# Performance work log

Measured on AMD Instinct MI355X. Metric: run time of the kernel, lower is better.

## Reference

```python
import jax, jax.numpy as jnp
import numpy as np

STEP, LEAK = 16, 32
KS = STEP + LEAK          # kernel_size = 48
FODEP = KS                # forced depression window
SYNAPSES, NEURONS = 64, 256
IC, OC = 1, 10
DENSE = 0.5
THETA = DENSE * SYNAPSES * IC   # 32.0
BIAS = 0.5
BATCH, TIME = 16, 512


def setup_inputs() -> dict:
    key = jax.random.key(0)
    k1, k2 = jax.random.split(key)
    # binary input spikes, density 0.2
    input_spikes = (jax.random.uniform(k1, (BATCH, IC, SYNAPSES, TIME)) < 0.2).astype(jnp.float32)
    # weight ~ Exponential(rate=1/w_init=2).sample().clip(0,1), mean 0.5
    u = jax.random.uniform(k2, (OC * NEURONS, IC * SYNAPSES), minval=1e-6, maxval=1.0)
    weight = jnp.clip(-0.5 * jnp.log(u), 0.0, 1.0)
    return {"input_spikes": input_spikes, "weight": weight}


def _step_fire_leak_kernel(weight):
    # kernel[o, i, t] = max(0, min(t/step, -(t - w*step)/leak + w)), flipped on t
    t = jnp.arange(KS, dtype=weight.dtype)
    t_spike = t / STEP                                        # rising edge
    t_leak = -(t - weight[..., None] * STEP) / LEAK + weight[..., None]  # decaying edge
    kernel = jnp.maximum(jnp.zeros((), weight.dtype), jnp.minimum(t_spike, t_leak))
    return kernel[..., ::-1]


def _forward(input_spikes, weight):
    B, C, S, T = input_spikes.shape
    x = input_spikes.reshape(B, C * S, T)
    kernel = _step_fire_leak_kernel(weight)                   # [OC*N, IC*S, KS]
    # conv1d with padding = kernel_size on both sides -> T' = T + KS + 1
    pot = jax.lax.conv_general_dilated(
        x, kernel, window_strides=(1,), padding=[(KS, KS)],
        dimension_numbers=("NCH", "OIH", "NCH"))
    Tp = pot.shape[-1]
    pot = pot.reshape(B, OC, NEURONS, Tp) + BIAS * THETA      # unsupervised bias path

    # winner-takes-all scan over time with per-(batch, neuron) depression counter
    pot_t = pot.transpose(3, 0, 2, 1)                         # [T', B, N, OC]
    dep0 = jnp.zeros((B, NEURONS, OC), jnp.int32)

    def step_fn(dep, p):
        masked = jnp.where(dep == 0, p, jnp.zeros((), p.dtype))
        winner = jnp.argmax(masked, axis=-1)                  # [B, N]
        wpot = jnp.take_along_axis(masked, winner[..., None], axis=-1)[..., 0]
        spike = (wpot > THETA).astype(p.dtype)                # [B, N]
        w_t = jax.nn.one_hot(winner, OC, dtype=p.dtype) * spike[..., None]
        dep = jnp.clip(dep + spike.astype(jnp.int32)[..., None] * FODEP - 1, 0, FODEP - 1)
        return dep, w_t

    _, winners = jax.lax.scan(step_fn, dep0, pot_t)           # [T', B, N, OC]
    return winners.transpose(1, 3, 2, 0)                      # [B, OC, N, T'] float


def reference(input_spikes, weight):
    return _forward(input_spikes, weight)
```

## Files before the change

### kernel.cpp

```cpp
#include <hip/hip_runtime.h>

#define B_   16
#define OC_  10
#define N_   256
#define O_   2560
#define S_   64
#define T_   512
#define KS_  48
#define TP_  561
#define TT   24
#define WROW 72

#define NOC   160
#define XROWS 624
#define JC    12
#define NPH   (KS_/JC)

using i32x4 = __attribute__((ext_vector_type(4))) int;

__global__ void prep_all(const float* __restrict__ x, const float* __restrict__ w,
                         unsigned char* __restrict__ xb, signed char* __restrict__ Bg) {
    if (blockIdx.x < 2048) {
        int idx = blockIdx.x * 256 + threadIdx.x;
        int t = idx & 511;
        int bi = idx >> 9;
        int i = bi & 63, b = bi >> 6;
        xb[((size_t)(b * 512 + t) << 6) + i] = (x[idx] != 0.0f) ? 1 : 0;
    } else {
        int idx = (blockIdx.x - 2048) * 256 + threadIdx.x;
        int i = idx & 63;
        int oj = idx >> 6;
        int j = oj % KS_, o = oj / KS_;
        float wv = w[(o << 6) + i];
        float rise = (float)j * 0.0625f;
        float leak = -((float)j - wv * 16.0f) * 0.03125f + wv;
        float kv   = fmaxf(0.0f, fminf(rise, leak));
        int q  = (int)lrintf(kv * 4194304.0f);
        int d0 = ((q + 128) & 255) - 128;
        int q1 = (q - d0) >> 8;
        int d1 = ((q1 + 128) & 255) - 128;
        int d2 = (q1 - d1) >> 8;
        int oc = o >> 4, ol = o & 15;
        int jm = j & 15, jh = j >> 4;
        int pos = (jm >> 2) * 12 + (jm & 3) * 3 + jh;
        int key = (ol >> 1) & 3;
        int bpos = ((((i >> 4) ^ key) << 4) | (i & 15));
        size_t base = (((size_t)(oc * KS_ + pos) * 48) + ol) * 64 + bpos;
        Bg[base]            = (signed char)d0;
        Bg[base + 16 * 64]  = (signed char)d1;
        Bg[base + 32 * 64]  = (signed char)d2;
    }
}

__global__ __launch_bounds__(256, 2) void gemm_i8(
    const unsigned char* __restrict__ xb,
    const signed char*  __restrict__ Bg,
    float* __restrict__ pot)
{
    __shared__ __align__(16) unsigned char xT[XROWS * 64];
    __shared__ __align__(16) signed char  Bst[JC * 48 * 64];

    const int tid  = threadIdx.x;
    const int lane = tid & 63;
    const int wave = tid >> 6;
    const int oc = blockIdx.x;
    const int b  = blockIdx.y;
    const int lrow = lane & 15;
    const int quad = lane >> 4;
    const int tw = wave * 144;
    const int coffB = ((quad ^ ((lrow >> 1) & 3)) << 4);

    const signed char* BgBase = Bg + (size_t)oc * KS_ * 48 * 64;

    auto stage = [&](int ph) {
        const signed char* src = BgBase + (size_t)(ph * JC) * 48 * 64;
        for (int c = tid; c < JC * 48 * 64 / 16; c += 256)
            __builtin_amdgcn_global_load_lds(
                (const __attribute__((address_space(1))) void*)(src + c * 16),
                (__attribute__((address_space(3))) void*)(Bst + c * 16),
                16, 0, 0);
    };

    stage(0);

    for (int z = tid; z < 112 * 4; z += 256) {
        int zi = z >> 2, p = z & 3;
        int r = (zi < 49) ? zi : (561 + zi - 49);
        *(i32x4*)(xT + r * 64 + p * 16) = (i32x4){0, 0, 0, 0};
    }
    const unsigned char* xbb = xb + ((size_t)b << 15);
    for (int q = tid; q < 2048; q += 256) {
        i32x4 v = *(const i32x4*)(xbb + q * 16);
        int t = q >> 2, p = q & 3;
        int r = 49 + t;
        *(i32x4*)(xT + r * 64 + ((p ^ ((r >> 1) & 3)) << 4)) = v;
    }

    i32x4 acc[9][3];
#pragma unroll
    for (int mi = 0; mi < 9; ++mi)
#pragma unroll
        for (int f = 0; f < 3; ++f)
            acc[mi][f] = (i32x4){0, 0, 0, 0};

    __syncthreads();

    for (int ph = 0; ph < NPH; ++ph) {
#pragma unroll
        for (int tloc = 0; tloc < 4; ++tloc) {
            const int j0 = ph * 4 + tloc;
            const int rb = tw + 16 - j0 + lrow;
            const int coffA = ((quad ^ ((rb >> 1) & 3)) << 4);
            i32x4 af[11], bf[3][3];
#pragma unroll
            for (int k = 0; k < 11; ++k)
                af[k] = *(const i32x4*)(xT + (rb + k * 16) * 64 + coffA);
#pragma unroll
            for (int jh = 0; jh < 3; ++jh)
#pragma unroll
                for (int f = 0; f < 3; ++f)
                    bf[jh][f] = *(const i32x4*)
                        (Bst + (((tloc * 3 + jh) * 48) + f * 16 + lrow) * 64 + coffB);
#pragma unroll
            for (int jh = 0; jh < 3; ++jh)
#pragma unroll
                for (int mi = 0; mi < 9; ++mi)
#pragma unroll
                    for (int f = 0; f < 3; ++f)
                        acc[mi][f] = __builtin_amdgcn_mfma_i32_16x16x64_i8(
                            af[mi + 2 - jh], bf[jh][f], acc[mi][f], 0, 0, 0);
        }
        __syncthreads();
        if (ph + 1 < NPH) {
            stage(ph + 1);
            __syncthreads();
        }
    }

    const size_t potb = (size_t)b * TP_;
#pragma unroll
    for (int mi = 0; mi < 9; ++mi) {
#pragma unroll
        for (int r = 0; r < 4; ++r) {
            int t = tw + mi * 16 + quad * 4 + r;
            if (t < TP_) {
                double pq = ((double)acc[mi][0][r]
                           + 256.0   * (double)acc[mi][1][r]
                           + 65536.0 * (double)acc[mi][2][r])
                          * (1.0 / 4194304.0);
                pot[(potb + t) * O_ + oc * 16 + lrow] = (float)pq;
            }
        }
    }
}

__global__ void transpose_w(const float* __restrict__ w, float* __restrict__ wT) {
    int idx = blockIdx.x * 256 + threadIdx.x;
    if (idx >= O_ * S_) return;
    int o = idx >> 6, i = idx & 63;
    wT[i * O_ + o] = w[idx];
}

__global__ __launch_bounds__(256) void conv_kernel(
    const float* __restrict__ x, const float* __restrict__ wT,
    float* __restrict__ pot)
{
    const int b  = blockIdx.y;
    const int t0 = blockIdx.z * TT;
    const int o  = blockIdx.x * 256 + threadIdx.x;

    __shared__ __align__(16) float xsh[S_][WROW];
    for (int idx = threadIdx.x; idx < S_ * WROW; idx += 256) {
        int i = idx / WROW, m = idx - i * WROW;
        int t = t0 - KS_ + m;
        float v = 0.0f;
        if (t >= 0 && t < T_) v = x[(b * S_ + i) * T_ + t];
        xsh[i][m] = v;
    }
    __syncthreads();

    float acch[TT], accl[TT];
#pragma unroll
    for (int tl = 0; tl < TT; ++tl) { acch[tl] = 0.0f; accl[tl] = 0.0f; }

    for (int i = 0; i < S_; ++i) {
        float xw[WROW];
#pragma unroll
        for (int w4 = 0; w4 < WROW / 4; ++w4) {
            const float4 v = *reinterpret_cast<const float4*>(&xsh[i][w4 * 4]);
            xw[w4 * 4 + 0] = v.x; xw[w4 * 4 + 1] = v.y;
            xw[w4 * 4 + 2] = v.z; xw[w4 * 4 + 3] = v.w;
        }
        const float wv = wT[i * O_ + o];
#pragma unroll
        for (int j = 1; j < KS_; ++j) {
            float rise = (float)j * 0.0625f;
            float leak = -((float)j - wv * 16.0f) * 0.03125f + wv;
            float kv   = fmaxf(0.0f, fminf(rise, leak));
            float khi  = rintf(kv * 4096.0f) * 2.44140625e-4f;
            float klo  = kv - khi;
#pragma unroll
            for (int tl = 0; tl < TT; ++tl) {
                float xv = xw[tl + (KS_ - 1) - j];
                acch[tl] = fmaf(xv, khi, acch[tl]);
                accl[tl] = fmaf(xv, klo, accl[tl]);
            }
        }
    }
#pragma unroll
    for (int tl = 0; tl < TT; ++tl) {
        int t = t0 + tl;
        if (t < TP_) pot[((size_t)b * TP_ + t) * O_ + o] = acch[tl] + accl[tl];
    }
}

__global__ void scan_prep(const float* __restrict__ pot, unsigned char* __restrict__ code) {
    int idx = blockIdx.x * 256 + threadIdx.x;
    if (idx >= B_ * TP_ * N_) return;
    int n  = idx & (N_ - 1);
    int bt = idx >> 8;
    const float* p = pot + (size_t)bt * O_ + n;
    float best = p[0]; int bo = 0;
#pragma unroll
    for (int oc = 1; oc < OC_; ++oc) {
        float v = p[oc * N_];
        if (v > best) { best = v; bo = oc; }
    }
    code[idx] = ((best + 16.0f) > 32.0f) ? (unsigned char)(bo + 1) : (unsigned char)0;
}

__global__ void scan_run(const unsigned char* __restrict__ code, float* __restrict__ out) {
    int idx = blockIdx.x * 256 + threadIdx.x;
    if (idx >= B_ * N_) return;
    int b = idx >> 8, n = idx & 255;
    const unsigned char* c = code + (size_t)b * TP_ * N_ + n;
    int t = 0;
    while (t < TP_) {
        unsigned char buf[KS_];
#pragma unroll
        for (int k = 0; k < KS_; ++k) {
            int tt = t + k;
            buf[k] = (tt < TP_) ? c[(size_t)tt * N_] : (unsigned char)0;
        }
        int adv = KS_;
#pragma unroll
        for (int k = 0; k < KS_; ++k) {
            if (buf[k]) {
                out[(((size_t)b * OC_ + (buf[k] - 1)) * N_ + n) * TP_ + (t + k)] = 1.0f;
                adv = k + KS_;
                break;
            }
        }
        t += adv;
    }
}

extern "C" void kernel_launch(void* const* d_in, const int* in_sizes, int n_in,
                              void* d_out, int out_size, void* d_ws, size_t ws_size,
                              hipStream_t stream) {
    const float* x = (const float*)d_in[0];
    const float* w = (const float*)d_in[1];
    float* out = (float*)d_out;

    char* ws = (char*)d_ws;
    const size_t szX = (size_t)B_ * T_ * S_;
    const size_t szB = (size_t)NOC * KS_ * 48 * 64;
    const size_t szP = (size_t)B_ * TP_ * O_ * 4;
    const size_t szC = (size_t)B_ * TP_ * N_;
    const size_t need = szX + szB + szP + szC;

    hipMemsetAsync(d_out, 0, (size_t)out_size * sizeof(float), stream);

    if (ws_size >= need) {
        unsigned char* xb  = (unsigned char*)ws;
        signed char* Bg    = (signed char*)(ws + szX);
        float* pot         = (float*)(ws + szX + szB);
        unsigned char* code = (unsigned char*)(ws + szX + szB + szP);

        prep_all<<<2048 + 30720, 256, 0, stream>>>(x, w, xb, Bg);
        gemm_i8<<<dim3(NOC, B_), 256, 0, stream>>>(xb, Bg, pot);
        scan_prep<<<(B_ * TP_ * N_ + 255) / 256, 256, 0, stream>>>(pot, code);
        scan_run<<<(B_ * N_ + 255) / 256, 256, 0, stream>>>(code, out);
    } else {
        size_t pot_bytes  = (size_t)B_ * TP_ * O_ * sizeof(float);
        size_t code_bytes = (size_t)B_ * TP_ * N_;
        float* pot = (float*)ws;
        unsigned char* code = (unsigned char*)(ws + pot_bytes);
        float* wT = (float*)(ws + pot_bytes + code_bytes);

        transpose_w<<<(O_ * S_ + 255) / 256, 256, 0, stream>>>(w, wT);
        conv_kernel<<<dim3(O_ / 256, B_, (TP_ + TT - 1) / TT), 256, 0, stream>>>(x, wT, pot);
        scan_prep<<<(B_ * TP_ * N_ + 255) / 256, 256, 0, stream>>>(pot, code);
        scan_run<<<(B_ * N_ + 255) / 256, 256, 0, stream>>>(code, out);
    }
}
```

Baseline: 283.1 us.

## Double-buffer weight staging in LDS and swap grid order for B reuse

Result: no change. 288.2 us (+1.8%).

```diff
diff --git a/kernel.cpp b/kernel.cpp
--- a/kernel.cpp
+++ b/kernel.cpp
@@ -13,7 +13,7 @@
 
 #define NOC   160
 #define XROWS 624
-#define JC    12
+#define JC    6
 #define NPH   (KS_/JC)
 
 using i32x4 = __attribute__((ext_vector_type(4))) int;
@@ -42,7 +42,7 @@
         int d2 = (q1 - d1) >> 8;
         int oc = o >> 4, ol = o & 15;
         int jm = j & 15, jh = j >> 4;
-        int pos = (jm >> 2) * 12 + (jm & 3) * 3 + jh;
+        int pos = jm * 3 + jh;
         int key = (ol >> 1) & 3;
         int bpos = ((((i >> 4) ^ key) << 4) | (i & 15));
         size_t base = (((size_t)(oc * KS_ + pos) * 48) + ol) * 64 + bpos;
@@ -58,13 +58,13 @@
     float* __restrict__ pot)
 {
     __shared__ __align__(16) unsigned char xT[XROWS * 64];
-    __shared__ __align__(16) signed char  Bst[JC * 48 * 64];
+    __shared__ __align__(16) signed char  Bst[2][JC * 48 * 64];
 
     const int tid  = threadIdx.x;
     const int lane = tid & 63;
     const int wave = tid >> 6;
-    const int oc = blockIdx.x;
-    const int b  = blockIdx.y;
+    const int b  = blockIdx.x;
+    const int oc = blockIdx.y;
     const int lrow = lane & 15;
     const int quad = lane >> 4;
     const int tw = wave * 144;
@@ -72,16 +72,17 @@
 
     const signed char* BgBase = Bg + (size_t)oc * KS_ * 48 * 64;
 
-    auto stage = [&](int ph) {
+    auto stage = [&](int ph, int buf) {
         const signed char* src = BgBase + (size_t)(ph * JC) * 48 * 64;
+        signed char* dst = &Bst[buf][0];
         for (int c = tid; c < JC * 48 * 64 / 16; c += 256)
             __builtin_amdgcn_global_load_lds(
                 (const __attribute__((address_space(1))) void*)(src + c * 16),
-                (__attribute__((address_space(3))) void*)(Bst + c * 16),
+                (__attribute__((address_space(3))) void*)(dst + c * 16),
                 16, 0, 0);
     };
 
-    stage(0);
+    stage(0, 0);
 
     for (int z = tid; z < 112 * 4; z += 256) {
         int zi = z >> 2, p = z & 3;
@@ -106,10 +107,14 @@
     __syncthreads();
 
     for (int ph = 0; ph < NPH; ++ph) {
-#pragma unroll
-        for (int tloc = 0; tloc < 4; ++tloc) {
-            const int j0 = ph * 4 + tloc;
-            const int rb = tw + 16 - j0 + lrow;
+        const int cur = ph & 1;
+        if (ph + 1 < NPH)
+            stage(ph + 1, 1 - cur);
+
+#pragma unroll
+        for (int tloc = 0; tloc < 2; ++tloc) {
+            const int g = ph * 2 + tloc;
+            const int rb = tw + 16 - g + lrow;
             const int coffA = ((quad ^ ((rb >> 1) & 3)) << 4);
             i32x4 af[11], bf[3][3];
 #pragma unroll
@@ -120,7 +125,7 @@
 #pragma unroll
                 for (int f = 0; f < 3; ++f)
                     bf[jh][f] = *(const i32x4*)
-                        (Bst + (((tloc * 3 + jh) * 48) + f * 16 + lrow) * 64 + coffB);
+                        (&Bst[cur][0] + (((tloc * 3 + jh) * 48) + f * 16 + lrow) * 64 + coffB);
 #pragma unroll
             for (int jh = 0; jh < 3; ++jh)
 #pragma unroll
@@ -131,10 +136,6 @@
                             af[mi + 2 - jh], bf[jh][f], acc[mi][f], 0, 0, 0);
         }
         __syncthreads();
-        if (ph + 1 < NPH) {
-            stage(ph + 1);
-            __syncthreads();
-        }
     }
 
     const size_t potb = (size_t)b * TP_;
@@ -278,7 +279,7 @@
         unsigned char* code = (unsigned char*)(ws + szX + szB + szP);
 
         prep_all<<<2048 + 30720, 256, 0, stream>>>(x, w, xb, Bg);
-        gemm_i8<<<dim3(NOC, B_), 256, 0, stream>>>(xb, Bg, pot);
+        gemm_i8<<<dim3(B_, NOC), 256, 0, stream>>>(xb, Bg, pot);
         scan_prep<<<(B_ * TP_ * N_ + 255) / 256, 256, 0, stream>>>(pot, code);
         scan_run<<<(B_ * N_ + 255) / 256, 256, 0, stream>>>(code, out);
     } else {
```

## Fuse scan prep and run into one kernel that writes the full dense output

Applied to the files above, without the earlier changes.

Result: faster. 270.7 us (-4.4%).

```diff
diff --git a/kernel.cpp b/kernel.cpp
--- a/kernel.cpp
+++ b/kernel.cpp
@@ -15,6 +15,8 @@
 #define XROWS 624
 #define JC    12
 #define NPH   (KS_/JC)
+
+#define CPITCH 572
 
 using i32x4 = __attribute__((ext_vector_type(4))) int;
 
@@ -154,6 +156,64 @@
     }
 }
 
+__global__ __launch_bounds__(256) void scan_fused(
+    const float* __restrict__ pot,
+    float* __restrict__ out)
+{
+    __shared__ unsigned char codeW[16 * CPITCH];
+    __shared__ unsigned char ocW[16 * CPITCH];
+
+    const int tid = threadIdx.x;
+    const int nc = blockIdx.x;
+    const int b  = blockIdx.y;
+    const int n0 = nc * 16;
+
+    for (int pair = tid; pair < TP_ * 16; pair += 256) {
+        int t = pair >> 4, nl = pair & 15;
+        const float* p = pot + ((size_t)(b * TP_ + t)) * O_ + n0 + nl;
+        float best = p[0]; int bo = 0;
+#pragma unroll
+        for (int ch = 1; ch < OC_; ++ch) {
+            float v = p[ch * N_];
+            if (v > best) { best = v; bo = ch; }
+        }
+        codeW[nl * CPITCH + t] =
+            ((best + 16.0f) > 32.0f) ? (unsigned char)(bo + 1) : (unsigned char)0;
+        ocW[nl * CPITCH + t] = 0;
+    }
+    __syncthreads();
+
+    if (tid < 16) {
+        const unsigned char* c = &codeW[tid * CPITCH];
+        unsigned char* o = &ocW[tid * CPITCH];
+        int t = 0;
+        while (t < TP_) {
+            unsigned char buf[KS_];
+#pragma unroll
+            for (int k = 0; k < KS_; ++k) {
+                int tt = t + k;
+                buf[k] = (tt < TP_) ? c[tt] : (unsigned char)0;
+            }
+            int adv = KS_;
+#pragma unroll
+            for (int k = 0; k < KS_; ++k) {
+                if (buf[k]) { o[t + k] = buf[k]; adv = k + KS_; break; }
+            }
+            t += adv;
+        }
+    }
+    __syncthreads();
+
+    float* ob = out + (((size_t)b * OC_) * N_ + n0) * TP_;
+    for (int idx = tid; idx < OC_ * 16 * TP_; idx += 256) {
+        int r = idx / TP_;
+        int t = idx - r * TP_;
+        int ch = r >> 4, nl = r & 15;
+        float v = (ocW[nl * CPITCH + t] == (unsigned char)(ch + 1)) ? 1.0f : 0.0f;
+        ob[((size_t)ch * N_ + nl) * TP_ + t] = v;
+    }
+}
+
 __global__ void transpose_w(const float* __restrict__ w, float* __restrict__ wT) {
     int idx = blockIdx.x * 256 + threadIdx.x;
     if (idx >= O_ * S_) return;
@@ -269,18 +329,14 @@
     const size_t szC = (size_t)B_ * TP_ * N_;
     const size_t need = szX + szB + szP + szC;
 
-    hipMemsetAsync(d_out, 0, (size_t)out_size * sizeof(float), stream);
-
     if (ws_size >= need) {
         unsigned char* xb  = (unsigned char*)ws;
         signed char* Bg    = (signed char*)(ws + szX);
         float* pot         = (float*)(ws + szX + szB);
-        unsigned char* code = (unsigned char*)(ws + szX + szB + szP);
 
         prep_all<<<2048 + 30720, 256, 0, stream>>>(x, w, xb, Bg);
         gemm_i8<<<dim3(NOC, B_), 256, 0, stream>>>(xb, Bg, pot);
-        scan_prep<<<(B_ * TP_ * N_ + 255) / 256, 256, 0, stream>>>(pot, code);
-        scan_run<<<(B_ * N_ + 255) / 256, 256, 0, stream>>>(code, out);
+        scan_fused<<<dim3(16, B_), 256, 0, stream>>>(pot, out);
     } else {
         size_t pot_bytes  = (size_t)B_ * TP_ * O_ * sizeof(float);
         size_t code_bytes = (size_t)B_ * TP_ * N_;
@@ -288,6 +344,7 @@
         unsigned char* code = (unsigned char*)(ws + pot_bytes);
         float* wT = (float*)(ws + pot_bytes + code_bytes);
 
+        hipMemsetAsync(d_out, 0, (size_t)out_size * sizeof(float), stream);
         transpose_w<<<(O_ * S_ + 255) / 256, 256, 0, stream>>>(w, wT);
         conv_kernel<<<dim3(O_ / 256, B_, (TP_ + TT - 1) / TT), 256, 0, stream>>>(x, wT, pot);
         scan_prep<<<(B_ * TP_ * N_ + 255) / 256, 256, 0, stream>>>(pot, code);
```
